# Kernel optimization log

Measured on AMD Instinct MI355X. Metric: run time of the kernel, lower is better.

Reference implementation:

```python
import jax, jax.numpy as jnp
import numpy as np

EMB, HEADS = 1024, 16
HD = EMB // HEADS


def setup_inputs() -> dict:
    key = jax.random.key(0)
    ks = jax.random.split(key, 9)
    B, T, C = 4, 2048, EMB
    s = 1.0 / np.sqrt(C)
    return {
        "x": jax.random.normal(ks[0], (B, T, C), jnp.float32),
        "Wq": jax.random.normal(ks[1], (C, C), jnp.float32) * s,
        "bq": jnp.zeros((C,), jnp.float32),
        "Wk": jax.random.normal(ks[2], (C, C), jnp.float32) * s,
        "bk": jnp.zeros((C,), jnp.float32),
        "Wv": jax.random.normal(ks[3], (C, C), jnp.float32) * s,
        "bv": jnp.zeros((C,), jnp.float32),
        "Wo": jax.random.normal(ks[4], (C, C), jnp.float32) * s,
        "bo": jnp.zeros((C,), jnp.float32),
    }


def _attn(x, Wq, bq, Wk, bk, Wv, bv, Wo, bo):
    B, T, C = x.shape
    # [B,T,C] -> [B,H,T,hd]
    def split(h):
        return h.reshape(B, T, HEADS, HD).transpose(0, 2, 1, 3)
    q = split(x @ Wq + bq)
    k = split(x @ Wk + bk)
    v = split(x @ Wv + bv)
    att = jnp.einsum("bhtd,bhsd->bhts", q, k) * (1.0 / np.sqrt(HD))
    causal = jnp.tril(jnp.ones((T, T), bool))  # [T,T]
    att = jnp.where(causal, att, -jnp.inf)
    att = jax.nn.softmax(att, axis=-1)
    y = jnp.einsum("bhts,bhsd->bhtd", att, v)
    y = y.transpose(0, 2, 1, 3).reshape(B, T, C)
    return y @ Wo + bo


def reference(x, Wq, bq, Wk, bk, Wv, bv, Wo, bo):
    return _attn(x, Wq, bq, Wk, bk, Wv, bv, Wo, bo)
```

## Files before the change

### kernel.cpp

```cpp
#include <hip/hip_runtime.h>
#include <cmath>

#define EMB 1024
#define HEADS 16
#define HD 64
#define BATCH 4
#define SEQ 2048
#define MTOT (BATCH * SEQ)

typedef __attribute__((ext_vector_type(8))) short short8;
typedef __attribute__((ext_vector_type(4))) float f32x4;
typedef __attribute__((ext_vector_type(16))) float f32x16;

__device__ __forceinline__ float b2f(unsigned short u) {
  union { unsigned int i; float f; } c; c.i = ((unsigned int)u) << 16; return c.f;
}
__device__ __forceinline__ unsigned short f2b(float f) {
  union { float f; unsigned int i; } c; c.f = f;
  unsigned int x = c.i;
  return (unsigned short)((x + 0x7fffu + ((x >> 16) & 1u)) >> 16);
}

#define GLD16(gp, lp) __builtin_amdgcn_global_load_lds( \
    (__attribute__((address_space(1))) unsigned int*)(gp), \
    (__attribute__((address_space(3))) unsigned int*)(lp), 16, 0, 0)

__global__ __launch_bounds__(256) void transpose_w4(
    const float* __restrict__ W0, const float* __restrict__ W1,
    const float* __restrict__ W2, const float* __restrict__ W3,
    unsigned short* __restrict__ Wt) {
  __shared__ float T[32][33];
  const int z = blockIdx.z;
  const float* W = (z == 0) ? W0 : (z == 1) ? W1 : (z == 2) ? W2 : W3;
  unsigned short* out = Wt + (size_t)z * EMB * EMB;
  const int k0 = blockIdx.x * 32, n0 = blockIdx.y * 32;
  const int tx = threadIdx.x, ty = threadIdx.y;
#pragma unroll
  for (int r = 0; r < 4; ++r)
    T[ty + r * 8][tx] = W[(size_t)(k0 + ty + r * 8) * EMB + n0 + tx];
  __syncthreads();
#pragma unroll
  for (int r = 0; r < 4; ++r)
    out[(size_t)(n0 + ty + r * 8) * EMB + k0 + tx] = f2b(T[tx][ty + r * 8]);
}

__global__ __launch_bounds__(256) void convert_x(
    const float* __restrict__ x, unsigned short* __restrict__ xb) {
  const size_t i = ((size_t)blockIdx.x * 256 + threadIdx.x) * 8;
  const float4 a = *(const float4*)(x + i);
  const float4 b = *(const float4*)(x + i + 4);
  ushort4 lo = {f2b(a.x), f2b(a.y), f2b(a.z), f2b(a.w)};
  ushort4 hi = {f2b(b.x), f2b(b.y), f2b(b.z), f2b(b.w)};
  *(ushort4*)(xb + i) = lo;
  *(ushort4*)(xb + i + 4) = hi;
}

template <int OUTMODE>
__global__ __launch_bounds__(256) void gemm_mfma(
    const unsigned short* __restrict__ A, const unsigned short* __restrict__ Bt,
    const float* __restrict__ bias, void* __restrict__ outp) {
  __shared__ unsigned short As[128 * 32];
  __shared__ unsigned short Bs[128 * 32];
  const int tid = threadIdx.x;
  const int w = tid >> 6, lane = tid & 63;
  const int g = lane >> 4, m = lane & 15;
  const int row0 = blockIdx.x * 128, col0 = blockIdx.y * 128;
  const int wm = (w >> 1) * 64, wn = (w & 1) * 64;

  f32x4 acc[4][4];
#pragma unroll
  for (int i = 0; i < 4; ++i)
#pragma unroll
    for (int j = 0; j < 4; ++j) acc[i][j] = (f32x4){0.f, 0.f, 0.f, 0.f};

  for (int kb = 0; kb < EMB; kb += 32) {
    if (kb) __syncthreads();
#pragma unroll
    for (int i = 0; i < 2; ++i) {
      const int segb = w * 64 + i * 256;
      const int seg = segb + lane;
      GLD16(Bt + (size_t)(col0 + (seg >> 2)) * EMB + kb + (seg & 3) * 8,
            &Bs[segb * 8]);
    }
#pragma unroll
    for (int i = 0; i < 2; ++i) {
      const int segb = w * 64 + i * 256;
      const int seg = segb + lane;
      GLD16(A + (size_t)(row0 + (seg >> 2)) * EMB + kb + (seg & 3) * 8,
            &As[segb * 8]);
    }
    __syncthreads();

    short8 af[4], bf[4];
#pragma unroll
    for (int i = 0; i < 4; ++i)
      af[i] = *(const short8*)&As[(wm + i * 16 + m) * 32 + g * 8];
#pragma unroll
    for (int j = 0; j < 4; ++j)
      bf[j] = *(const short8*)&Bs[(wn + j * 16 + m) * 32 + g * 8];
#pragma unroll
    for (int i = 0; i < 4; ++i)
#pragma unroll
      for (int j = 0; j < 4; ++j)
        acc[i][j] = __builtin_amdgcn_mfma_f32_16x16x32_bf16(af[i], bf[j],
                                                            acc[i][j], 0, 0, 0);
  }

  float bv[4];
#pragma unroll
  for (int j = 0; j < 4; ++j) bv[j] = bias[col0 + wn + j * 16 + m];

#pragma unroll
  for (int i = 0; i < 4; ++i)
#pragma unroll
    for (int j = 0; j < 4; ++j)
#pragma unroll
      for (int r = 0; r < 4; ++r) {
        const size_t row = row0 + wm + i * 16 + g * 4 + r;
        const size_t col = col0 + wn + j * 16 + m;
        const float val = acc[i][j][r] + bv[j];
        if constexpr (OUTMODE == 0) ((float*)outp)[row * EMB + col] = val;
        else ((unsigned short*)outp)[row * EMB + col] = f2b(val);
      }
}

__global__ __launch_bounds__(256) void gemm_qkv(
    const unsigned short* __restrict__ A, const unsigned short* __restrict__ Wt,
    const float* __restrict__ b0, const float* __restrict__ b1,
    const float* __restrict__ b2, unsigned short* __restrict__ out) {
  __shared__ unsigned short As[128 * 32];
  __shared__ unsigned short Bs[128 * 32];
  const int z = blockIdx.z;
  const unsigned short* Bt = Wt + (size_t)z * EMB * EMB;
  const float* bias = (z == 0) ? b0 : ((z == 1) ? b1 : b2);
  const int tid = threadIdx.x;
  const int w = tid >> 6, lane = tid & 63;
  const int g = lane >> 4, m = lane & 15;
  const int row0 = blockIdx.x * 128, col0 = blockIdx.y * 128;
  const int wm = (w >> 1) * 64, wn = (w & 1) * 64;

  f32x4 acc[4][4];
#pragma unroll
  for (int i = 0; i < 4; ++i)
#pragma unroll
    for (int j = 0; j < 4; ++j) acc[i][j] = (f32x4){0.f, 0.f, 0.f, 0.f};

  for (int kb = 0; kb < EMB; kb += 32) {
    if (kb) __syncthreads();
#pragma unroll
    for (int i = 0; i < 2; ++i) {
      const int segb = w * 64 + i * 256;
      const int seg = segb + lane;
      GLD16(Bt + (size_t)(col0 + (seg >> 2)) * EMB + kb + (seg & 3) * 8,
            &Bs[segb * 8]);
    }
#pragma unroll
    for (int i = 0; i < 2; ++i) {
      const int segb = w * 64 + i * 256;
      const int seg = segb + lane;
      GLD16(A + (size_t)(row0 + (seg >> 2)) * EMB + kb + (seg & 3) * 8,
            &As[segb * 8]);
    }
    __syncthreads();

    short8 af[4], bf[4];
#pragma unroll
    for (int i = 0; i < 4; ++i)
      af[i] = *(const short8*)&As[(wm + i * 16 + m) * 32 + g * 8];
#pragma unroll
    for (int j = 0; j < 4; ++j)
      bf[j] = *(const short8*)&Bs[(wn + j * 16 + m) * 32 + g * 8];
#pragma unroll
    for (int i = 0; i < 4; ++i)
#pragma unroll
      for (int j = 0; j < 4; ++j)
        acc[i][j] = __builtin_amdgcn_mfma_f32_16x16x32_bf16(af[i], bf[j],
                                                            acc[i][j], 0, 0, 0);
  }

  float bv[4];
#pragma unroll
  for (int j = 0; j < 4; ++j) bv[j] = bias[col0 + wn + j * 16 + m];

  if (z == 2) {
    unsigned short* Vt = out + (size_t)2 * MTOT * EMB;
    const int bi = row0 >> 11;
    const int tb = (row0 & 2047) + wm;
#pragma unroll
    for (int i = 0; i < 4; ++i)
#pragma unroll
      for (int j = 0; j < 4; ++j) {
        const int col = col0 + wn + j * 16 + m;
        const int t0 = tb + i * 16 + g * 4;
        ushort4 pv = {f2b(acc[i][j][0] + bv[j]), f2b(acc[i][j][1] + bv[j]),
                      f2b(acc[i][j][2] + bv[j]), f2b(acc[i][j][3] + bv[j])};
        *(ushort4*)&Vt[(size_t)(bi * 1024 + col) * SEQ + t0] = pv;
      }
  } else {
    unsigned short* O = out + (size_t)z * MTOT * EMB;
#pragma unroll
    for (int i = 0; i < 4; ++i)
#pragma unroll
      for (int j = 0; j < 4; ++j)
#pragma unroll
        for (int r = 0; r < 4; ++r) {
          const size_t row = row0 + wm + i * 16 + g * 4 + r;
          const size_t col = col0 + wn + j * 16 + m;
          O[row * EMB + col] = f2b(acc[i][j][r] + bv[j]);
        }
  }
}

__global__ __launch_bounds__(512, 4) void flash_mfma(
    const unsigned short* __restrict__ Qg, const unsigned short* __restrict__ Kg,
    const unsigned short* __restrict__ Vtg, unsigned short* __restrict__ Yg) {
  __shared__ unsigned short Kl[2][64 * 64];
  __shared__ unsigned short Vl[2][64 * 64];
  const int tid = threadIdx.x;
  const int w = tid >> 6, lane = tid & 63;
  const int ql = lane & 31;
  const int hi = lane >> 5;

  const int gid = blockIdx.x;
  const int low3 = gid & 7, mid3 = (gid >> 3) & 7;
  const int hi2 = (gid >> 6) & 3, half = gid >> 8;
  const int qb = half ? mid3 : 7 - mid3;
  const int hb = low3 | (hi2 << 3) | (half << 5);
  const int bi = hb >> 4, hd = hb & 15;

  const size_t base = ((size_t)bi * SEQ) * EMB + (size_t)hd * HD;
  const size_t vtrow0 = (size_t)(bi * HEADS + hd) * HD;

  const int r8 = lane >> 3;
  const int c8 = ((lane & 7) ^ r8) * 8;

#define STAGE(tile_, buf_)                                                  \
  do {                                                                      \
    const int s0_ = (tile_) * 64;                                           \
    GLD16(Kg + base + (size_t)(s0_ + 8 * w + r8) * EMB + c8,                \
          &Kl[buf_][(8 * w) * 64]);                                         \
    GLD16(Vtg + (vtrow0 + 8 * w + r8) * SEQ + s0_ + c8,                     \
          &Vl[buf_][(8 * w) * 64]);                                         \
  } while (0)

  const int q0w = qb * 256 + 32 * w;
  const int q = q0w + ql;

  short8 qf[4];
#pragma unroll
  for (int s = 0; s < 4; ++s) {
    const uint4 u = *(const uint4*)(
        Qg + base + (size_t)q * EMB + s * 16 + hi * 8);
    const unsigned short* t = (const unsigned short*)&u;
    short8 qv;
#pragma unroll
    for (int j = 0; j < 8; ++j) qv[j] = (short)f2b(b2f(t[j]) * 0.125f);
    qf[s] = qv;
  }

  f32x16 acc[2];
#pragma unroll
  for (int db = 0; db < 2; ++db)
#pragma unroll
    for (int i = 0; i < 16; ++i) acc[db][i] = 0.f;
  float m_r = -INFINITY, l_r = 0.f;

  const int nt = 4 * qb + 4;
  STAGE(0, 0);

  int buf = 0;
  for (int t = 0; t < nt; ++t) {
    asm volatile("s_waitcnt vmcnt(0)" ::: "memory");
    __builtin_amdgcn_s_barrier();
    if (t + 1 < nt) STAGE(t + 1, buf ^ 1);
    const int s0 = t * 64;
    if (s0 <= q0w + 31) {
      const unsigned short* K0 = Kl[buf];
      const unsigned short* V0 = Vl[buf];

      f32x16 sA[2];
#pragma unroll
      for (int n = 0; n < 2; ++n) {
        const int row = 32 * n + ql;
        const int rb = row * 64, rk = row & 7;
        f32x16 z;
#pragma unroll
        for (int i = 0; i < 16; ++i) z[i] = 0.f;
#pragma unroll
        for (int s = 0; s < 4; ++s) {
          const short8 kf =
              *(const short8*)&K0[rb + (((2 * s + hi) ^ rk) * 8)];
          z = __builtin_amdgcn_mfma_f32_32x32x16_bf16(kf, qf[s], z, 0, 0, 0);
        }
        sA[n] = z;
      }

      if (s0 + 63 > q) {
#pragma unroll
        for (int n = 0; n < 2; ++n)
#pragma unroll
          for (int r = 0; r < 16; ++r)
            if (s0 + 32 * n + (r & 3) + 8 * (r >> 2) + 4 * hi > q)
              sA[n][r] = -INFINITY;
      }

      float tmax = -INFINITY;
#pragma unroll
      for (int n = 0; n < 2; ++n)
#pragma unroll
        for (int r = 0; r < 16; ++r) tmax = fmaxf(tmax, sA[n][r]);
      tmax = fmaxf(tmax, __shfl_xor(tmax, 32));

      if (!__all(tmax - m_r <= 8.f)) {
        const float nm = fmaxf(m_r, tmax);
        const float sc = __expf(m_r - nm);
#pragma unroll
        for (int db = 0; db < 2; ++db)
#pragma unroll
          for (int i = 0; i < 16; ++i) acc[db][i] *= sc;
        l_r *= sc;
        m_r = nm;
      }

      float ps = 0.f;
#pragma unroll
      for (int n = 0; n < 2; ++n)
#pragma unroll
        for (int r = 0; r < 16; ++r) {
          const float p = __expf(sA[n][r] - m_r);
          sA[n][r] = p;
          ps += p;
        }
      ps += __shfl_xor(ps, 32);
      l_r += ps;

      unsigned int pk[2][8];
#pragma unroll
      for (int n = 0; n < 2; ++n)
#pragma unroll
        for (int i = 0; i < 8; ++i) {
          unsigned int d;
          asm("v_cvt_pk_bf16_f32 %0, %1, %2"
              : "=v"(d) : "v"(sA[n][2 * i]), "v"(sA[n][2 * i + 1]));
          pk[n][i] = d;
        }
      union { unsigned int u[4]; short8 s; } pf[4];
#pragma unroll
      for (int ks = 0; ks < 4; ++ks) {
        const int n = ks >> 1, k4 = (ks & 1) * 4;
        unsigned int a0 = pk[n][k4 + 0], a1 = pk[n][k4 + 1];
        unsigned int b0 = pk[n][k4 + 2], b1 = pk[n][k4 + 3];
        asm("v_permlane32_swap_b32 %0, %1" : "+v"(a0), "+v"(b0));
        asm("v_permlane32_swap_b32 %0, %1" : "+v"(a1), "+v"(b1));
        pf[ks].u[0] = a0; pf[ks].u[1] = a1;
        pf[ks].u[2] = b0; pf[ks].u[3] = b1;
      }

#pragma unroll
      for (int db = 0; db < 2; ++db) {
        const int row = 32 * db + ql;
        const int rb = row * 64, rk = row & 7;
#pragma unroll
        for (int ks = 0; ks < 4; ++ks) {
          const short8 vf =
              *(const short8*)&V0[rb + (((2 * ks + hi) ^ rk) * 8)];
          acc[db] = __builtin_amdgcn_mfma_f32_32x32x16_bf16(vf, pf[ks].s,
                                                            acc[db], 0, 0, 0);
        }
      }
    }
    buf ^= 1;
  }

  const float iv = 1.f / l_r;
  unsigned short* Yrow = Yg + base + (size_t)q * EMB;
#pragma unroll
  for (int db = 0; db < 2; ++db)
#pragma unroll
    for (int r = 0; r < 16; r += 2) {
      unsigned int d;
      const float lo = acc[db][r] * iv, hh = acc[db][r + 1] * iv;
      asm("v_cvt_pk_bf16_f32 %0, %1, %2" : "=v"(d) : "v"(lo), "v"(hh));
      const int col = 32 * db + (r & 3) + 8 * (r >> 2) + 4 * hi;
      *(unsigned int*)(Yrow + col) = d;
    }
#undef STAGE
}

extern "C" void kernel_launch(void* const* d_in, const int* in_sizes, int n_in,
                              void* d_out, int out_size, void* d_ws, size_t ws_size,
                              hipStream_t stream) {
  const float* x  = (const float*)d_in[0];
  const float* Wq = (const float*)d_in[1];
  const float* bq = (const float*)d_in[2];
  const float* Wk = (const float*)d_in[3];
  const float* bk = (const float*)d_in[4];
  const float* Wv = (const float*)d_in[5];
  const float* bv = (const float*)d_in[6];
  const float* Wo = (const float*)d_in[7];
  const float* bo = (const float*)d_in[8];
  float* out = (float*)d_out;

  unsigned short* wqt = (unsigned short*)d_ws;
  unsigned short* wot = wqt + (size_t)3 * EMB * EMB;
  unsigned short* Q  = wqt + (size_t)4 * EMB * EMB;
  unsigned short* K  = Q + (size_t)MTOT * EMB;
  unsigned short* Vt = K + (size_t)MTOT * EMB;
  unsigned short* Y  = Vt + (size_t)MTOT * EMB;
  unsigned short* xb = Y + (size_t)MTOT * EMB;

  transpose_w4<<<dim3(EMB / 32, EMB / 32, 4), dim3(32, 8), 0, stream>>>(
      Wq, Wk, Wv, Wo, wqt);
  convert_x<<<dim3(MTOT * EMB / (256 * 8)), 256, 0, stream>>>(x, xb);

  gemm_qkv<<<dim3(MTOT / 128, EMB / 128, 3), 256, 0, stream>>>(
      xb, wqt, bq, bk, bv, Q);
  flash_mfma<<<dim3(512), 512, 0, stream>>>(Q, K, Vt, Y);
  gemm_mfma<0><<<dim3(MTOT / 128, EMB / 128), 256, 0, stream>>>(
      Y, wot, bo, out);
}
```

Before: 169.8 us.

## Halve flash attention block size, remap grid, use exp2 and MFMA priority hints

The flash attention kernel now uses 256-thread blocks covering 128 queries each, launched as 1024 blocks with a new block-to-(head, query-block) mapping that interleaves heavy and light causal blocks. Each warp stages two K/V row groups, since there are half as many warps. The softmax switches to raw v_exp_f32 (base-2) with log2(e) folded into the Q scale, the rescale threshold is raised to match, and s_setprio brackets the MFMA sections. The aim is better load balance and occupancy plus cheaper exponentials, at the cost of more blocks re-reading K/V tiles.

```diff
diff --git a/kernel.cpp b/kernel.cpp
--- a/kernel.cpp
+++ b/kernel.cpp
@@ -211,7 +211,7 @@
   }
 }
 
-__global__ __launch_bounds__(512, 4) void flash_mfma(
+__global__ __launch_bounds__(256, 4) void flash_mfma(
     const unsigned short* __restrict__ Qg, const unsigned short* __restrict__ Kg,
     const unsigned short* __restrict__ Vtg, unsigned short* __restrict__ Yg) {
   __shared__ unsigned short Kl[2][64 * 64];
@@ -222,10 +222,11 @@
   const int hi = lane >> 5;
 
   const int gid = blockIdx.x;
-  const int low3 = gid & 7, mid3 = (gid >> 3) & 7;
-  const int hi2 = (gid >> 6) & 3, half = gid >> 8;
-  const int qb = half ? mid3 : 7 - mid3;
-  const int hb = low3 | (hi2 << 3) | (half << 5);
+  const int g2 = gid & 3;
+  const int hb = (gid >> 2) & 63;
+  const int g8 = gid >> 8;
+  const int q4 = g2 * 4 + g8;
+  const int qb = (q4 & 1) ? (q4 >> 1) : (15 - (q4 >> 1));
   const int bi = hb >> 4, hd = hb & 15;
 
   const size_t base = ((size_t)bi * SEQ) * EMB + (size_t)hd * HD;
@@ -237,13 +238,21 @@
 #define STAGE(tile_, buf_)                                                  \
   do {                                                                      \
     const int s0_ = (tile_) * 64;                                           \
-    GLD16(Kg + base + (size_t)(s0_ + 8 * w + r8) * EMB + c8,                \
-          &Kl[buf_][(8 * w) * 64]);                                         \
-    GLD16(Vtg + (vtrow0 + 8 * w + r8) * SEQ + s0_ + c8,                     \
-          &Vl[buf_][(8 * w) * 64]);                                         \
+    _Pragma("unroll")                                                       \
+    for (int L = 0; L < 2; ++L) {                                           \
+      const int rb_ = 16 * w + 8 * L;                                       \
+      GLD16(Kg + base + (size_t)(s0_ + rb_ + r8) * EMB + c8,                \
+            &Kl[buf_][rb_ * 64]);                                           \
+    }                                                                       \
+    _Pragma("unroll")                                                       \
+    for (int L = 0; L < 2; ++L) {                                           \
+      const int rb_ = 16 * w + 8 * L;                                       \
+      GLD16(Vtg + (vtrow0 + rb_ + r8) * SEQ + s0_ + c8,                     \
+            &Vl[buf_][rb_ * 64]);                                           \
+    }                                                                       \
   } while (0)
 
-  const int q0w = qb * 256 + 32 * w;
+  const int q0w = qb * 128 + 32 * w;
   const int q = q0w + ql;
 
   short8 qf[4];
@@ -254,7 +263,7 @@
     const unsigned short* t = (const unsigned short*)&u;
     short8 qv;
 #pragma unroll
-    for (int j = 0; j < 8; ++j) qv[j] = (short)f2b(b2f(t[j]) * 0.125f);
+    for (int j = 0; j < 8; ++j) qv[j] = (short)f2b(b2f(t[j]) * 0.18033688f);
     qf[s] = qv;
   }
 
@@ -265,7 +274,7 @@
     for (int i = 0; i < 16; ++i) acc[db][i] = 0.f;
   float m_r = -INFINITY, l_r = 0.f;
 
-  const int nt = 4 * qb + 4;
+  const int nt = 2 * qb + 2;
   STAGE(0, 0);
 
   int buf = 0;
@@ -279,6 +288,7 @@
       const unsigned short* V0 = Vl[buf];
 
       f32x16 sA[2];
+      __builtin_amdgcn_s_setprio(1);
 #pragma unroll
       for (int n = 0; n < 2; ++n) {
         const int row = 32 * n + ql;
@@ -294,6 +304,7 @@
         }
         sA[n] = z;
       }
+      __builtin_amdgcn_s_setprio(0);
 
       if (s0 + 63 > q) {
 #pragma unroll
@@ -311,9 +322,11 @@
         for (int r = 0; r < 16; ++r) tmax = fmaxf(tmax, sA[n][r]);
       tmax = fmaxf(tmax, __shfl_xor(tmax, 32));
 
-      if (!__all(tmax - m_r <= 8.f)) {
+      if (!__all(tmax - m_r <= 11.f)) {
         const float nm = fmaxf(m_r, tmax);
-        const float sc = __expf(m_r - nm);
+        float sc;
+        const float d0 = m_r - nm;
+        asm("v_exp_f32 %0, %1" : "=v"(sc) : "v"(d0));
 #pragma unroll
         for (int db = 0; db < 2; ++db)
 #pragma unroll
@@ -327,7 +340,9 @@
       for (int n = 0; n < 2; ++n)
 #pragma unroll
         for (int r = 0; r < 16; ++r) {
-          const float p = __expf(sA[n][r] - m_r);
+          float p;
+          const float d1 = sA[n][r] - m_r;
+          asm("v_exp_f32 %0, %1" : "=v"(p) : "v"(d1));
           sA[n][r] = p;
           ps += p;
         }
@@ -356,6 +371,7 @@
         pf[ks].u[2] = b0; pf[ks].u[3] = b1;
       }
 
+      __builtin_amdgcn_s_setprio(1);
 #pragma unroll
       for (int db = 0; db < 2; ++db) {
         const int row = 32 * db + ql;
@@ -368,6 +384,7 @@
                                                             acc[db], 0, 0, 0);
         }
       }
+      __builtin_amdgcn_s_setprio(0);
     }
     buf ^= 1;
   }
@@ -415,7 +432,7 @@
 
   gemm_qkv<<<dim3(MTOT / 128, EMB / 128, 3), 256, 0, stream>>>(
       xb, wqt, bq, bk, bv, Q);
-  flash_mfma<<<dim3(512), 512, 0, stream>>>(Q, K, Vt, Y);
+  flash_mfma<<<dim3(1024), 256, 0, stream>>>(Q, K, Vt, Y);
   gemm_mfma<0><<<dim3(MTOT / 128, EMB / 128), 256, 0, stream>>>(
       Y, wot, bo, out);
 }
```

After: 163.1 us. 1.04x faster.
